# Optimization experiments

Hardware: AMD Instinct MI355X
Metric: run time of the kernel (lower is better)

The kernel has to match this reference:

```python
import jax, jax.numpy as jnp
import numpy as np

B, MB, NB, C = 4, 4096, 16384, 64

def setup_inputs() -> dict:
    key = jax.random.key(0)
    k1, k2, k3 = jax.random.split(key, 3)
    xyz = jax.random.normal(k1, (B * MB, 3), dtype=jnp.float32) * 10.0
    new_xyz = jax.random.normal(k2, (B * NB, 3), dtype=jnp.float32) * 10.0
    features = jax.random.normal(k3, (B * MB, C), dtype=jnp.float32)
    xyz_batch_cnt = jnp.full((B,), MB, dtype=jnp.int32)
    new_xyz_batch_cnt = jnp.full((B,), NB, dtype=jnp.int32)
    return {
        "xyz": xyz,
        "xyz_batch_cnt": xyz_batch_cnt,
        "new_xyz": new_xyz,
        "new_xyz_batch_cnt": new_xyz_batch_cnt,
        "features": features,
    }

def _three_nn_interp(query, known, feats):
    # query: (Nb,3), known: (Mb,3), feats: (Mb,C)
    # squared pairwise distances (Nb, Mb)
    d2 = (jnp.sum(query * query, -1, keepdims=True)
          - 2.0 * (query @ known.T)
          + jnp.sum(known * known, -1)[None, :])
    neg_d2, idx = jax.lax.top_k(-d2, 3)            # 3 nearest, (Nb,3)
    dist = jnp.sqrt(jnp.maximum(-neg_d2, 0.0))      # OpenPCDet returns sqrt(dist2)
    dist_recip = 1.0 / (dist + 1e-8)
    weight = dist_recip / jnp.sum(dist_recip, -1, keepdims=True)  # (Nb,3)
    gathered = feats[idx]                           # (Nb,3,C)
    return jnp.einsum('nkc,nk->nc', gathered, weight)

def reference(xyz, xyz_batch_cnt, new_xyz, new_xyz_batch_cnt, features):
    b = xyz_batch_cnt.shape[0]
    mb = xyz.shape[0] // b
    nb = new_xyz.shape[0] // b
    known_b = xyz.reshape(b, mb, 3)
    query_b = new_xyz.reshape(b, nb, 3)
    feats_b = features.reshape(b, mb, -1)
    out = jax.vmap(_three_nn_interp)(query_b, known_b, feats_b)  # (B,Nb,C)
    return out.reshape(b * nb, -1)
```

## Files before the change

kernel.cpp:

```cpp
#include <hip/hip_runtime.h>
#include <math.h>

#define NBIN   512
#define BEXT   64.0f
#define WSLACK 0.02f
#define AWIN   4.0f
#define SLC    64
#define BTH1   1024

__device__ __forceinline__ int bin1(float x) {
    int c = (int)floorf((x + BEXT) * 4.0f);
    return min(NBIN - 1, max(0, c));
}
__device__ __forceinline__ unsigned f2sort(float f) {
    int b = __float_as_int(f);
    return (unsigned)b ^ (0x80000000u | (unsigned)(b >> 31));
}
__device__ __forceinline__ float sort2f(unsigned u) {
    unsigned b = (u & 0x80000000u) ? (u ^ 0x80000000u) : ~u;
    return __uint_as_float(b);
}
__device__ __forceinline__ void ins3k(unsigned long long k,
                                      unsigned long long& k0,
                                      unsigned long long& k1,
                                      unsigned long long& k2) {
    const bool c0 = k < k0, c1 = k < k1, c2 = k < k2;
    k2 = c1 ? k1 : (c2 ? k : k2);
    k1 = c0 ? k0 : (c1 ? k : k1);
    k0 = c0 ? k  : k0;
}
__device__ __forceinline__ unsigned long long shfl_xor_u64(unsigned long long v, int m) {
    unsigned lo = (unsigned)v, hi = (unsigned)(v >> 32);
    lo = __shfl_xor((int)lo, m, 64);
    hi = __shfl_xor((int)hi, m, 64);
    return ((unsigned long long)hi << 32) | lo;
}

extern "C" __global__ void __launch_bounds__(256)
k_shist(const float* __restrict__ xyz, const float* __restrict__ nxyz,
        int B, int mb, int nb,
        int* __restrict__ hP, int* __restrict__ hQ, int* __restrict__ ovf_cnt)
{
    __shared__ int hist[NBIN];
    const int bid = (int)blockIdx.x;
    const bool isQ = bid >= B * SLC;
    const int rb = isQ ? bid - B * SLC : bid;
    const int b = rb / SLC, s = rb % SLC;
    const int n = isQ ? nb : mb;
    const int len = (n + SLC - 1) / SLC;
    const int beg = s * len, end = min(n, beg + len);
    const float* P = (isQ ? nxyz : xyz) + (size_t)b * n * 3;
    const int tid = threadIdx.x;

    if (bid == 0 && tid < B) ovf_cnt[tid] = 0;

    for (int i = tid; i < NBIN; i += 256) hist[i] = 0;
    __syncthreads();
    for (int i = beg + tid; i < end; i += 256) atomicAdd(&hist[bin1(P[i * 3])], 1);
    __syncthreads();
    int* dst = (isQ ? hQ : hP) + ((size_t)b * SLC + s) * NBIN;
    for (int i = tid; i < NBIN; i += 256) dst[i] = hist[i];
}

extern "C" __global__ void __launch_bounds__(NBIN)
k_sscan(int* __restrict__ hP, int* __restrict__ hQ,
        int* __restrict__ boff, int B, int mb)
{
    __shared__ int sc[NBIN];
    const bool isQ = (int)blockIdx.x >= B;
    const int b = isQ ? (int)blockIdx.x - B : (int)blockIdx.x;
    int* h = (isQ ? hQ : hP) + (size_t)b * SLC * NBIN;
    const int c = threadIdx.x;

    int run = 0;
    for (int s = 0; s < SLC; ++s) {
        const int v = h[s * NBIN + c];
        h[s * NBIN + c] = run;
        run += v;
    }
    sc[c] = run;
    __syncthreads();
    for (int off = 1; off < NBIN; off <<= 1) {
        const int t = (c >= off) ? sc[c - off] : 0;
        __syncthreads();
        sc[c] += t;
        __syncthreads();
    }
    const int excl = sc[c] - run;
    for (int s = 0; s < SLC; ++s) h[s * NBIN + c] += excl;
    if (!isQ) {
        boff[(size_t)b * (NBIN + 1) + c] = excl;
        if (c == NBIN - 1) boff[(size_t)b * (NBIN + 1) + NBIN] = mb;
    }
}

extern "C" __global__ void __launch_bounds__(256)
k_sscat(const float* __restrict__ xyz, const float* __restrict__ nxyz,
        int B, int mb, int nb,
        const int* __restrict__ hP, const int* __restrict__ hQ,
        float4* __restrict__ ps, int* __restrict__ pidx, int* __restrict__ qord)
{
    __shared__ int cur[NBIN];
    const int bid = (int)blockIdx.x;
    const bool isQ = bid >= B * SLC;
    const int rb = isQ ? bid - B * SLC : bid;
    const int b = rb / SLC, s = rb % SLC;
    const int n = isQ ? nb : mb;
    const int len = (n + SLC - 1) / SLC;
    const int beg = s * len, end = min(n, beg + len);
    const float* P = (isQ ? nxyz : xyz) + (size_t)b * n * 3;
    const int tid = threadIdx.x;
    const int* src = (isQ ? hQ : hP) + ((size_t)b * SLC + s) * NBIN;

    for (int i = tid; i < NBIN; i += 256) cur[i] = src[i];
    __syncthreads();
    for (int i = beg + tid; i < end; i += 256) {
        const float x = P[i * 3], y = P[i * 3 + 1], z = P[i * 3 + 2];
        const int pos = atomicAdd(&cur[bin1(x)], 1);
        if (isQ) {
            qord[(size_t)b * nb + pos] = i;
        } else {
            float pn;
            {
#pragma clang fp contract(off)
                pn = (x * x + y * y) + z * z;
            }
            ps[(size_t)b * mb + pos]   = make_float4(x, y, z, pn);
            pidx[(size_t)b * mb + pos] = i;
        }
    }
}

extern "C" __global__ void __launch_bounds__(BTH1)
build1d(const float* __restrict__ xyz, const float* __restrict__ nxyz,
        int mb, int nb,
        float4* __restrict__ ps, int* __restrict__ pidx,
        int* __restrict__ qord, int* __restrict__ boff,
        int* __restrict__ ovf_cnt)
{
    __shared__ int hist[NBIN];
    __shared__ int scanb[NBIN];
    const int B    = (int)gridDim.x / 2;
    const bool isQ = (int)blockIdx.x >= B;
    const int b    = isQ ? (int)blockIdx.x - B : (int)blockIdx.x;
    const int tid  = threadIdx.x;
    const int n    = isQ ? nb : mb;
    const float* P = (isQ ? nxyz : xyz) + (size_t)b * n * 3;

    if (blockIdx.x == 0 && tid < B) ovf_cnt[tid] = 0;

    if (tid < NBIN) hist[tid] = 0;
    __syncthreads();
    for (int i = tid; i < n; i += BTH1) atomicAdd(&hist[bin1(P[i * 3])], 1);
    __syncthreads();
    int h = 0;
    if (tid < NBIN) { h = hist[tid]; scanb[tid] = h; }
    __syncthreads();
    for (int off = 1; off < NBIN; off <<= 1) {
        int t = 0;
        if (tid < NBIN && tid >= off) t = scanb[tid - off];
        __syncthreads();
        if (tid < NBIN) scanb[tid] += t;
        __syncthreads();
    }
    if (tid < NBIN) {
        const int excl = scanb[tid] - h;
        if (!isQ) {
            boff[(size_t)b * (NBIN + 1) + tid] = excl;
            if (tid == NBIN - 1) boff[(size_t)b * (NBIN + 1) + NBIN] = n;
        }
        hist[tid] = excl;
    }
    __syncthreads();
    for (int i = tid; i < n; i += BTH1) {
        const float x = P[i * 3], y = P[i * 3 + 1], z = P[i * 3 + 2];
        const int c = bin1(x);
        const int pos = atomicAdd(&hist[c], 1);
        if (isQ) {
            qord[(size_t)b * nb + pos] = i;
        } else {
            float pn;
            {
#pragma clang fp contract(off)
                pn = (x * x + y * y) + z * z;
            }
            ps[(size_t)b * mb + pos]   = make_float4(x, y, z, pn);
            pidx[(size_t)b * mb + pos] = i;
        }
    }
}

#define QWA  8
#define SWA  8
#define WVBA 4
#define WTHA (WVBA * 64)
#define QPBA (WVBA * QWA)
#define CHA  64

extern "C" __global__ void __launch_bounds__(WTHA)
knn_phaseA(const float* __restrict__ nxyz, const float* __restrict__ feats,
           const int* __restrict__ qord, const int* __restrict__ boff,
           const float4* __restrict__ ps, const int* __restrict__ pidx,
           float* __restrict__ out, int* __restrict__ ovf, float* __restrict__ ovf_ub,
           int* __restrict__ ovf_cnt, int mb, int nb, int C)
{
    __shared__ float4 sP[WVBA][CHA];
    __shared__ int    sI[WVBA][CHA];

    const int tid  = threadIdx.x;
    const int w    = tid >> 6;
    const int l    = tid & 63;
    const int qi   = l & 7;
    const int side = l >> 3;
    const int wid  = blockIdx.x * WVBA + w;
    const int q0   = wid * QWA;
    const int b    = q0 / nb;

    const int qloc = qord[q0 + qi];
    const int row  = b * nb + qloc;
    const float qx = nxyz[(size_t)row * 3 + 0];
    const float qy = nxyz[(size_t)row * 3 + 1];
    const float qz = nxyz[(size_t)row * 3 + 2];
    float qq;
    {
#pragma clang fp contract(off)
        qq = (qx * qx + qy * qy) + qz * qz;
    }

    float mn = qx, mx = qx;
#pragma unroll
    for (int m = 1; m < 64; m <<= 1) {
        mn = fminf(mn, __shfl_xor(mn, m, 64));
        mx = fmaxf(mx, __shfl_xor(mx, m, 64));
    }

    const int*    boffb = boff + (size_t)b * (NBIN + 1);
    const float4* psb   = ps   + (size_t)b * mb;
    const int*    pib   = pidx + (size_t)b * mb;

    unsigned long long k0 = ~0ull, k1 = ~0ull, k2 = ~0ull;

    float4 rP;
    int    rI = 0;
    bool   rV = false;
    auto issue = [&](int base, int hi) {
        const int cand = base + l;
        rV = cand < hi;
        if (rV) { rP = psb[cand]; rI = pib[cand]; }
    };
    auto commit = [&]() {
        if (rV) { sP[w][l] = rP; sI[w][l] = rI; }
    };
    auto process = [&](int cnt) {
#pragma unroll
        for (int u = 0; u < CHA / SWA; ++u) {
            const int j = side + u * SWA;
            if (j < cnt) {
                const float4 Pt = sP[w][j];
                const int    pi = sI[w][j];
                const float dot = fmaf(qz, Pt.z, fmaf(qy, Pt.y, qx * Pt.x));
                const float d2  = fmaf(-2.0f, dot, qq) + Pt.w;
                const unsigned long long key =
                    ((unsigned long long)f2sort(d2) << 32) | (unsigned)pi;
                if (key < k2) {
                    const bool c0 = key < k0, c1 = key < k1;
                    k2 = c1 ? k1 : key;
                    k1 = c0 ? k0 : (c1 ? key : k1);
                    k0 = c0 ? key : k0;
                }
            }
        }
    };

    const int blo = bin1(mn - AWIN);
    const int bhi = bin1(mx + AWIN);
    {
        const int lo = boffb[blo], hi = boffb[bhi + 1];
        if (lo < hi) {
            issue(lo, hi);
            for (int base = lo; base < hi; base += CHA) {
                commit();
                if (base + CHA < hi) issue(base + CHA, hi);
                process(min(CHA, hi - base));
            }
        }
    }

    unsigned long long m0 = k0, m1 = k1, m2 = k2;
#pragma unroll
    for (int mk = 8; mk <= 32; mk <<= 1) {
        const unsigned long long t0 = shfl_xor_u64(m0, mk);
        const unsigned long long t1 = shfl_xor_u64(m1, mk);
        const unsigned long long t2 = shfl_xor_u64(m2, mk);
        ins3k(t0, m0, m1, m2); ins3k(t1, m0, m1, m2); ins3k(t2, m0, m1, m2);
    }

    const unsigned h2 = (unsigned)(m2 >> 32);
    const float ub = (h2 == 0xFFFFFFFFu) ? INFINITY : sort2f(h2);
    const float eL = fmaf(0.25f, (float)blo, -BEXT);
    const float eR = fmaf(0.25f, (float)(bhi + 1), -BEXT);
    const float gL = qx - eL;
    const float gR = eR - qx;
    const bool okL = (blo == 0)        || (gL * gL > ub + WSLACK);
    const bool okR = (bhi >= NBIN - 1) || (gR * gR > ub + WSLACK);
    const bool resolved = okL && okR && (h2 != 0xFFFFFFFFu);

    const bool need = (side == 0) && !resolved;
    const unsigned long long bm = __ballot(need);
    if (bm) {
        const int rank = __popcll(bm & ((1ull << l) - 1ull));
        const int tot  = __popcll(bm);
        const int lead = __ffsll((unsigned long long)bm) - 1;
        int base = 0;
        if (l == lead) base = atomicAdd(&ovf_cnt[b], tot);
        base = __shfl(base, lead, 64);
        if (need) {
            ovf[(size_t)b * nb + base + rank]    = row;
            ovf_ub[(size_t)b * nb + base + rank] = ub;
        }
    }

    const float d0  = sort2f((unsigned)(m0 >> 32));
    const float d1  = sort2f((unsigned)(m1 >> 32));
    const float d2v = sort2f((unsigned)(m2 >> 32));
    const float da = sqrtf(fmaxf(d0, 0.0f));
    const float db = sqrtf(fmaxf(d1, 0.0f));
    const float dc = sqrtf(fmaxf(d2v, 0.0f));
    const float ra = 1.0f / (da + 1e-8f);
    const float rb = 1.0f / (db + 1e-8f);
    const float rc = 1.0f / (dc + 1e-8f);
    float rs;
    {
#pragma clang fp contract(off)
        rs = (ra + rb) + rc;
    }
    const float wa = ra / rs, wb = rb / rs, wc = rc / rs;
    const int   ia = b * mb + (int)(unsigned)(m0 & 0xFFFFFFFFu);
    const int   ib = b * mb + (int)(unsigned)(m1 & 0xFFFFFFFFu);
    const int   ic = b * mb + (int)(unsigned)(m2 & 0xFFFFFFFFu);

    for (int q = 0; q < QWA; ++q) {
        if (__shfl((int)resolved, q, 64) == 0) continue;
        const float wa_ = __shfl(wa, q, 64);
        const float wb_ = __shfl(wb, q, 64);
        const float wc_ = __shfl(wc, q, 64);
        const int   ia_ = __shfl(ia, q, 64);
        const int   ib_ = __shfl(ib, q, 64);
        const int   ic_ = __shfl(ic, q, 64);
        const int   rw_ = __shfl(row, q, 64);
        const size_t ga = (size_t)ia_ * C;
        const size_t gb = (size_t)ib_ * C;
        const size_t gc = (size_t)ic_ * C;
        const size_t go = (size_t)rw_ * C;
        for (int ch = l; ch < C; ch += 64) {
            out[go + ch] = wa_ * feats[ga + ch] + wb_ * feats[gb + ch] + wc_ * feats[gc + ch];
        }
    }
}

#define WPBB 8
#define BTH2 (WPBB * 64)

extern "C" __global__ void __launch_bounds__(BTH2)
knn_phaseB2(const float* __restrict__ nxyz, const float* __restrict__ feats,
            const int* __restrict__ ovf, const float* __restrict__ ovf_ub,
            const int* __restrict__ ovf_cnt, const int* __restrict__ boff,
            const float4* __restrict__ ps, const int* __restrict__ pidx,
            float* __restrict__ out, int mb, int nb, int C)
{
    const int tid  = threadIdx.x;
    const int w    = tid >> 6;
    const int l    = tid & 63;
    const int bpb  = nb / WPBB;
    const int bb   = (int)blockIdx.x / bpb;
    const int slot = ((int)blockIdx.x % bpb) * WPBB + w;
    const int cnt  = ovf_cnt[bb];
    if (slot >= cnt) return;

    const int   row = ovf[(size_t)bb * nb + slot];
    const float ub  = ovf_ub[(size_t)bb * nb + slot];
    const float qx = nxyz[(size_t)row * 3 + 0];
    const float qy = nxyz[(size_t)row * 3 + 1];
    const float qz = nxyz[(size_t)row * 3 + 2];
    float qq;
    {
#pragma clang fp contract(off)
        qq = (qx * qx + qy * qy) + qz * qz;
    }

    int blo = 0, bhi = NBIN - 1;
    if (ub < 1e30f) {
        const float r = sqrtf(ub + 2.0f * WSLACK);
        blo = bin1(qx - r);
        bhi = bin1(qx + r);
    }
    const int*    boffb = boff + (size_t)bb * (NBIN + 1);
    const float4* psb   = ps   + (size_t)bb * mb;
    const int*    pib   = pidx + (size_t)bb * mb;
    const int lo = boffb[blo], hi = boffb[bhi + 1];

    unsigned long long k0 = ~0ull, k1 = ~0ull, k2 = ~0ull;
#pragma unroll 4
    for (int t = lo + l; t < hi; t += 64) {
        const float4 Pt = psb[t];
        const int    pi = pib[t];
        const float dot = fmaf(qz, Pt.z, fmaf(qy, Pt.y, qx * Pt.x));
        const float d2  = fmaf(-2.0f, dot, qq) + Pt.w;
        const unsigned long long key =
            ((unsigned long long)f2sort(d2) << 32) | (unsigned)pi;
        if (key < k2) {
            const bool c0 = key < k0, c1 = key < k1;
            k2 = c1 ? k1 : key;
            k1 = c0 ? k0 : (c1 ? key : k1);
            k0 = c0 ? key : k0;
        }
    }

#pragma unroll
    for (int m = 1; m < 64; m <<= 1) {
        const unsigned long long t0 = shfl_xor_u64(k0, m);
        const unsigned long long t1 = shfl_xor_u64(k1, m);
        const unsigned long long t2 = shfl_xor_u64(k2, m);
        ins3k(t0, k0, k1, k2); ins3k(t1, k0, k1, k2); ins3k(t2, k0, k1, k2);
    }

    const float d0  = sort2f((unsigned)(k0 >> 32));
    const float d1  = sort2f((unsigned)(k1 >> 32));
    const float d2v = sort2f((unsigned)(k2 >> 32));
    const float da = sqrtf(fmaxf(d0, 0.0f));
    const float db = sqrtf(fmaxf(d1, 0.0f));
    const float dc = sqrtf(fmaxf(d2v, 0.0f));
    const float ra = 1.0f / (da + 1e-8f);
    const float rb = 1.0f / (db + 1e-8f);
    const float rc = 1.0f / (dc + 1e-8f);
    float rs;
    {
#pragma clang fp contract(off)
        rs = (ra + rb) + rc;
    }
    const float wa = ra / rs, wb = rb / rs, wc = rc / rs;
    const size_t ga = (size_t)(bb * mb + (int)(unsigned)(k0 & 0xFFFFFFFFu)) * C;
    const size_t gb = (size_t)(bb * mb + (int)(unsigned)(k1 & 0xFFFFFFFFu)) * C;
    const size_t gc = (size_t)(bb * mb + (int)(unsigned)(k2 & 0xFFFFFFFFu)) * C;
    const size_t go = (size_t)row * C;
    for (int ch = l; ch < C; ch += 64) {
        out[go + ch] = wa * feats[ga + ch] + wb * feats[gb + ch] + wc * feats[gc + ch];
    }
}

#define THREADS 512
#define WAVES   8
#define RQ      2
#define QPB     128
#define CHUNK   2048

extern "C" __global__ void __launch_bounds__(THREADS)
knn3_v5(const float* __restrict__ xyz,
        const float* __restrict__ new_xyz,
        const float* __restrict__ feats,
        float* __restrict__ out,
        int mb, int nb, int C)
{
    extern __shared__ float smem[];
    float4* s_pts = (float4*)smem;
    const int tid = threadIdx.x;
    const int w   = tid >> 6;
    const int l   = tid & 63;
    const int block_q0 = blockIdx.x * QPB;
    const int batch    = block_q0 / nb;
    const int known0   = batch * mb;

    float qx[RQ], qy[RQ], qz[RQ], qq[RQ];
#pragma unroll
    for (int r = 0; r < RQ; ++r) {
        const int gq = block_q0 + r * 64 + l;
        qx[r] = new_xyz[(size_t)gq * 3 + 0];
        qy[r] = new_xyz[(size_t)gq * 3 + 1];
        qz[r] = new_xyz[(size_t)gq * 3 + 2];
        {
#pragma clang fp contract(off)
            qq[r] = (qx[r] * qx[r] + qy[r] * qy[r]) + qz[r] * qz[r];
        }
    }
    float b0[RQ], b1[RQ], b2[RQ];
    int   i0[RQ], i1[RQ], i2[RQ];
#pragma unroll
    for (int r = 0; r < RQ; ++r) {
        b0[r] = INFINITY; b1[r] = INFINITY; b2[r] = INFINITY;
        i0[r] = 0; i1[r] = 0; i2[r] = 0;
    }
    const int nch = (mb + CHUNK - 1) / CHUNK;
    for (int c = 0; c < nch; ++c) {
        const int base = c * CHUNK;
        const int cnt  = min(CHUNK, mb - base);
        if (c > 0) __syncthreads();
        const float* src = xyz + (size_t)(known0 + base) * 3;
        for (int p = tid; p < cnt; p += THREADS) {
            const float px = src[p * 3 + 0];
            const float py = src[p * 3 + 1];
            const float pz = src[p * 3 + 2];
            float pn;
            {
#pragma clang fp contract(off)
                pn = (px * px + py * py) + pz * pz;
            }
            s_pts[p] = make_float4(px, py, pz, pn);
        }
        __syncthreads();
        const int lo = (w * cnt) / WAVES;
        const int hi = ((w + 1) * cnt) / WAVES;
#pragma unroll 4
        for (int p = lo; p < hi; ++p) {
            const float4 P = s_pts[p];
            const int gp = base + p;
#pragma unroll
            for (int r = 0; r < RQ; ++r) {
                const float dot = fmaf(qz[r], P.z, fmaf(qy[r], P.y, qx[r] * P.x));
                const float d2  = fmaf(-2.0f, dot, qq[r]) + P.w;
                const bool c0 = d2 < b0[r];
                const bool c1 = d2 < b1[r];
                const bool c2 = d2 < b2[r];
                const float n0 = fminf(d2, b0[r]);
                const float n1 = __builtin_amdgcn_fmed3f(d2, b0[r], b1[r]);
                const float n2 = __builtin_amdgcn_fmed3f(d2, b1[r], b2[r]);
                const int  j0 = c0 ? gp : i0[r];
                const int  j1 = c0 ? i0[r] : (c1 ? gp : i1[r]);
                const int  j2 = c1 ? i1[r] : (c2 ? gp : i2[r]);
                b0[r] = n0; b1[r] = n1; b2[r] = n2;
                i0[r] = j0; i1[r] = j1; i2[r] = j2;
            }
        }
    }
    __syncthreads();
    float* sB  = smem;
    int*   sI  = (int*)smem + 3 * WAVES * QPB;
    float* sFW = smem + 6 * WAVES * QPB;
    int*   sFI = (int*)sFW + 3 * QPB;
#pragma unroll
    for (int r = 0; r < RQ; ++r) {
        const int qb = r * 64 + l;
        sB[(0 * WAVES + w) * QPB + qb] = b0[r];
        sB[(1 * WAVES + w) * QPB + qb] = b1[r];
        sB[(2 * WAVES + w) * QPB + qb] = b2[r];
        sI[(0 * WAVES + w) * QPB + qb] = i0[r];
        sI[(1 * WAVES + w) * QPB + qb] = i1[r];
        sI[(2 * WAVES + w) * QPB + qb] = i2[r];
    }
    __syncthreads();
    if (tid < QPB) {
        float mv0 = sB[(0 * WAVES) * QPB + tid];
        float mv1 = sB[(1 * WAVES) * QPB + tid];
        float mv2 = sB[(2 * WAVES) * QPB + tid];
        int   mi0 = sI[(0 * WAVES) * QPB + tid];
        int   mi1 = sI[(1 * WAVES) * QPB + tid];
        int   mi2 = sI[(2 * WAVES) * QPB + tid];
        for (int c = 1; c < WAVES; ++c) {
#pragma unroll
            for (int kk = 0; kk < 3; ++kk) {
                const float x  = sB[(kk * WAVES + c) * QPB + tid];
                const int   xi = sI[(kk * WAVES + c) * QPB + tid];
                const bool c0 = (x < mv0) || (x == mv0 && xi < mi0);
                const bool c1 = (x < mv1) || (x == mv1 && xi < mi1);
                const bool c2 = (x < mv2) || (x == mv2 && xi < mi2);
                const float n2 = c1 ? mv1 : (c2 ? x : mv2);
                const int   j2 = c1 ? mi1 : (c2 ? xi : mi2);
                const float n1 = c0 ? mv0 : (c1 ? x : mv1);
                const int   j1 = c0 ? mi0 : (c1 ? xi : mi1);
                const float n0 = c0 ? x : mv0;
                const int   j0 = c0 ? xi : mi0;
                mv0 = n0; mv1 = n1; mv2 = n2;
                mi0 = j0; mi1 = j1; mi2 = j2;
            }
        }
        const float da = sqrtf(fmaxf(mv0, 0.0f));
        const float db = sqrtf(fmaxf(mv1, 0.0f));
        const float dc = sqrtf(fmaxf(mv2, 0.0f));
        const float ra = 1.0f / (da + 1e-8f);
        const float rb = 1.0f / (db + 1e-8f);
        const float rc = 1.0f / (dc + 1e-8f);
        float rsum;
        {
#pragma clang fp contract(off)
            rsum = (ra + rb) + rc;
        }
        sFW[0 * QPB + tid] = ra / rsum;
        sFW[1 * QPB + tid] = rb / rsum;
        sFW[2 * QPB + tid] = rc / rsum;
        sFI[0 * QPB + tid] = known0 + mi0;
        sFI[1 * QPB + tid] = known0 + mi1;
        sFI[2 * QPB + tid] = known0 + mi2;
    }
    __syncthreads();
    const int qpw = QPB / WAVES;
    for (int j = 0; j < qpw; ++j) {
        const int qi2 = w * qpw + j;
        const float wa = sFW[0 * QPB + qi2];
        const float wb = sFW[1 * QPB + qi2];
        const float wc = sFW[2 * QPB + qi2];
        const size_t ga = (size_t)sFI[0 * QPB + qi2] * C;
        const size_t gb = (size_t)sFI[1 * QPB + qi2] * C;
        const size_t gc = (size_t)sFI[2 * QPB + qi2] * C;
        const size_t go = (size_t)(block_q0 + qi2) * C;
        for (int ch = l; ch < C; ch += 64) {
            out[go + ch] = wa * feats[ga + ch] + wb * feats[gb + ch] + wc * feats[gc + ch];
        }
    }
}

#define FQPB 256
extern "C" __global__ void __launch_bounds__(FQPB)
knn3_fallback(const float* __restrict__ xyz,
              const float* __restrict__ new_xyz,
              const float* __restrict__ feats,
              float* __restrict__ out,
              int mb, int nb, int C)
{
    extern __shared__ float4 s_pts[];
    const int tid      = threadIdx.x;
    const int block_q0 = blockIdx.x * FQPB;
    const int batch    = block_q0 / nb;
    const int known0   = batch * mb;
    for (int p = tid; p < mb; p += FQPB) {
        const float px = xyz[(size_t)(known0 + p) * 3 + 0];
        const float py = xyz[(size_t)(known0 + p) * 3 + 1];
        const float pz = xyz[(size_t)(known0 + p) * 3 + 2];
        float pn;
        {
#pragma clang fp contract(off)
            pn = (px * px + py * py) + pz * pz;
        }
        s_pts[p] = make_float4(px, py, pz, pn);
    }
    __syncthreads();
    const int gq = block_q0 + tid;
    const float qx = new_xyz[(size_t)gq * 3 + 0];
    const float qy = new_xyz[(size_t)gq * 3 + 1];
    const float qz = new_xyz[(size_t)gq * 3 + 2];
    float qq;
    {
#pragma clang fp contract(off)
        qq = (qx * qx + qy * qy) + qz * qz;
    }
    float b0 = INFINITY, b1 = INFINITY, b2 = INFINITY;
    int   i0 = 0, i1 = 0, i2 = 0;
#pragma unroll 8
    for (int p = 0; p < mb; ++p) {
        const float4 P = s_pts[p];
        const float dot = fmaf(qz, P.z, fmaf(qy, P.y, qx * P.x));
        const float d2  = fmaf(-2.0f, dot, qq) + P.w;
        const bool c0 = d2 < b0;
        const bool c1 = d2 < b1;
        const bool c2 = d2 < b2;
        b2 = c1 ? b1 : (c2 ? d2 : b2);
        i2 = c1 ? i1 : (c2 ? p  : i2);
        b1 = c0 ? b0 : (c1 ? d2 : b1);
        i1 = c0 ? i0 : (c1 ? p  : i1);
        b0 = c0 ? d2 : b0;
        i0 = c0 ? p  : i0;
    }
    const float da = sqrtf(fmaxf(b0, 0.0f));
    const float db = sqrtf(fmaxf(b1, 0.0f));
    const float dc = sqrtf(fmaxf(b2, 0.0f));
    const float ra = 1.0f / (da + 1e-8f);
    const float rb = 1.0f / (db + 1e-8f);
    const float rc = 1.0f / (dc + 1e-8f);
    float rsum;
    {
#pragma clang fp contract(off)
        rsum = (ra + rb) + rc;
    }
    const float wa = ra / rsum, wb = rb / rsum, wc = rc / rsum;
    const size_t ga = (size_t)(known0 + i0) * C;
    const size_t gb = (size_t)(known0 + i1) * C;
    const size_t gc = (size_t)(known0 + i2) * C;
    const size_t go = (size_t)gq * C;
    for (int ch = 0; ch < C; ++ch) {
        out[go + ch] = wa * feats[ga + ch] + wb * feats[gb + ch] + wc * feats[gc + ch];
    }
}

extern "C" void kernel_launch(void* const* d_in, const int* in_sizes, int n_in,
                              void* d_out, int out_size, void* d_ws, size_t ws_size,
                              hipStream_t stream) {
    const float* xyz     = (const float*)d_in[0];
    const float* new_xyz = (const float*)d_in[2];
    const float* feats   = (const float*)d_in[4];
    float*       out     = (float*)d_out;

    const int n_known = in_sizes[0] / 3;
    const int B       = in_sizes[1];
    const int n_query = in_sizes[2] / 3;
    const int C       = in_sizes[4] / n_known;
    const int mb      = n_known / B;
    const int nb      = n_query / B;

    char* wp = (char*)d_ws;
    float4* ps      = (float4*)wp;  wp += (size_t)B * mb * sizeof(float4);
    int*    pidx    = (int*)wp;     wp += (size_t)B * mb * sizeof(int);
    int*    qord    = (int*)wp;     wp += (size_t)B * nb * sizeof(int);
    int*    boff    = (int*)wp;     wp += (size_t)B * (NBIN + 1) * sizeof(int);
    int*    ovf     = (int*)wp;     wp += (size_t)B * nb * sizeof(int);
    float*  ovf_ub  = (float*)wp;   wp += (size_t)B * nb * sizeof(float);
    int*    ovf_cnt = (int*)wp;     wp += (size_t)B * sizeof(int);
    const size_t need_base = (size_t)(wp - (char*)d_ws);
    int*    hP      = (int*)wp;     wp += (size_t)B * SLC * NBIN * sizeof(int);
    int*    hQ      = (int*)wp;     wp += (size_t)B * SLC * NBIN * sizeof(int);
    const size_t need_slice = (size_t)(wp - (char*)d_ws);

    const bool ok_shape = (nb % QWA) == 0 && (n_query % QPBA) == 0 &&
                          (nb % WPBB) == 0 && mb >= 3 && B <= 256;

    if (ok_shape && ws_size >= need_slice) {
        k_shist<<<2 * B * SLC, 256, 0, stream>>>(xyz, new_xyz, B, mb, nb, hP, hQ, ovf_cnt);
        k_sscan<<<2 * B, NBIN, 0, stream>>>(hP, hQ, boff, B, mb);
        k_sscat<<<2 * B * SLC, 256, 0, stream>>>(xyz, new_xyz, B, mb, nb, hP, hQ,
                                                 ps, pidx, qord);
        knn_phaseA<<<n_query / QPBA, WTHA, 0, stream>>>(
            new_xyz, feats, qord, boff, ps, pidx, out, ovf, ovf_ub, ovf_cnt,
            mb, nb, C);
        knn_phaseB2<<<B * (nb / WPBB), BTH2, 0, stream>>>(
            new_xyz, feats, ovf, ovf_ub, ovf_cnt, boff, ps, pidx, out, mb, nb, C);
    } else if (ok_shape && ws_size >= need_base && B <= BTH1) {
        build1d<<<2 * B, BTH1, 0, stream>>>(xyz, new_xyz, mb, nb, ps, pidx, qord,
                                            boff, ovf_cnt);
        knn_phaseA<<<n_query / QPBA, WTHA, 0, stream>>>(
            new_xyz, feats, qord, boff, ps, pidx, out, ovf, ovf_ub, ovf_cnt,
            mb, nb, C);
        knn_phaseB2<<<B * (nb / WPBB), BTH2, 0, stream>>>(
            new_xyz, feats, ovf, ovf_ub, ovf_cnt, boff, ps, pidx, out, mb, nb, C);
    } else if ((nb % QPB) == 0) {
        const size_t smem_chunk = (size_t)CHUNK * sizeof(float4);
        const size_t smem_merge = (size_t)(6 * WAVES * QPB + 6 * QPB) * sizeof(float);
        const size_t shmem = smem_chunk > smem_merge ? smem_chunk : smem_merge;
        knn3_v5<<<n_query / QPB, THREADS, shmem, stream>>>(
            xyz, new_xyz, feats, out, mb, nb, C);
    } else {
        const size_t shmem = (size_t)mb * sizeof(float4);
        knn3_fallback<<<(n_query + FQPB - 1) / FQPB, FQPB, shmem, stream>>>(
            xyz, new_xyz, feats, out, mb, nb, C);
    }
}
```

Baseline: 97.00 us.

## Replace 1D x-binning with 2D x/y grid for candidate search

```diff
diff --git a/kernel.cpp b/kernel.cpp
--- a/kernel.cpp
+++ b/kernel.cpp
@@ -1,16 +1,24 @@
 #include <hip/hip_runtime.h>
 #include <math.h>
 
-#define NBIN   512
-#define BEXT   64.0f
+#define NXB    256
+#define NYS    32
+#define NB2    (NYS * NXB)
 #define WSLACK 0.02f
-#define AWIN   4.0f
-#define SLC    64
-#define BTH1   1024
-
-__device__ __forceinline__ int bin1(float x) {
-    int c = (int)floorf((x + BEXT) * 4.0f);
-    return min(NBIN - 1, max(0, c));
+#define WX     3.0f
+#define WY     3.0f
+#define SLC2   8
+
+__device__ __forceinline__ int xbin(float x) {
+    int c = (int)floorf((x + 64.0f) * 2.0f);
+    return min(NXB - 1, max(0, c));
+}
+__device__ __forceinline__ int ybin(float y) {
+    int c = (int)floorf((y + 64.0f) * 0.25f);
+    return min(NYS - 1, max(0, c));
+}
+__device__ __forceinline__ int key2(float x, float y) {
+    return ybin(y) * NXB + xbin(x);
 }
 __device__ __forceinline__ unsigned f2sort(float f) {
     int b = __float_as_int(f);
@@ -37,86 +45,99 @@
 }
 
 extern "C" __global__ void __launch_bounds__(256)
-k_shist(const float* __restrict__ xyz, const float* __restrict__ nxyz,
-        int B, int mb, int nb,
-        int* __restrict__ hP, int* __restrict__ hQ, int* __restrict__ ovf_cnt)
+k_shist2(const float* __restrict__ xyz, const float* __restrict__ nxyz,
+         int B, int mb, int nb,
+         int* __restrict__ hP, int* __restrict__ hQ, int* __restrict__ ovf_cnt)
 {
-    __shared__ int hist[NBIN];
+    __shared__ int hist[NB2];
     const int bid = (int)blockIdx.x;
-    const bool isQ = bid >= B * SLC;
-    const int rb = isQ ? bid - B * SLC : bid;
-    const int b = rb / SLC, s = rb % SLC;
+    const bool isQ = bid >= B * SLC2;
+    const int rb = isQ ? bid - B * SLC2 : bid;
+    const int b = rb / SLC2, s = rb % SLC2;
     const int n = isQ ? nb : mb;
-    const int len = (n + SLC - 1) / SLC;
+    const int len = (n + SLC2 - 1) / SLC2;
     const int beg = s * len, end = min(n, beg + len);
     const float* P = (isQ ? nxyz : xyz) + (size_t)b * n * 3;
     const int tid = threadIdx.x;
 
     if (bid == 0 && tid < B) ovf_cnt[tid] = 0;
 
-    for (int i = tid; i < NBIN; i += 256) hist[i] = 0;
-    __syncthreads();
-    for (int i = beg + tid; i < end; i += 256) atomicAdd(&hist[bin1(P[i * 3])], 1);
-    __syncthreads();
-    int* dst = (isQ ? hQ : hP) + ((size_t)b * SLC + s) * NBIN;
-    for (int i = tid; i < NBIN; i += 256) dst[i] = hist[i];
-}
-
-extern "C" __global__ void __launch_bounds__(NBIN)
-k_sscan(int* __restrict__ hP, int* __restrict__ hQ,
-        int* __restrict__ boff, int B, int mb)
+    for (int i = tid; i < NB2; i += 256) hist[i] = 0;
+    __syncthreads();
+    for (int i = beg + tid; i < end; i += 256)
+        atomicAdd(&hist[key2(P[i * 3], P[i * 3 + 1])], 1);
+    __syncthreads();
+    int* dst = (isQ ? hQ : hP) + ((size_t)b * SLC2 + s) * NB2;
+    for (int i = tid; i < NB2; i += 256) dst[i] = hist[i];
+}
+
+extern "C" __global__ void __launch_bounds__(512)
+k_sscan2(int* __restrict__ hP, int* __restrict__ hQ,
+         int* __restrict__ boff, int B, int mb)
 {
-    __shared__ int sc[NBIN];
+    __shared__ int ts[512];
     const bool isQ = (int)blockIdx.x >= B;
     const int b = isQ ? (int)blockIdx.x - B : (int)blockIdx.x;
-    int* h = (isQ ? hQ : hP) + (size_t)b * SLC * NBIN;
-    const int c = threadIdx.x;
-
-    int run = 0;
-    for (int s = 0; s < SLC; ++s) {
-        const int v = h[s * NBIN + c];
-        h[s * NBIN + c] = run;
-        run += v;
-    }
-    sc[c] = run;
-    __syncthreads();
-    for (int off = 1; off < NBIN; off <<= 1) {
-        const int t = (c >= off) ? sc[c - off] : 0;
+    int* h = (isQ ? hQ : hP) + (size_t)b * SLC2 * NB2;
+    const int t = threadIdx.x;
+
+    int tot[16];
+    int tsum = 0;
+#pragma unroll
+    for (int j = 0; j < 16; ++j) {
+        const int c = t * 16 + j;
+        int run = 0;
+        for (int s = 0; s < SLC2; ++s) {
+            const int v = h[s * NB2 + c];
+            h[s * NB2 + c] = run;
+            run += v;
+        }
+        tot[j] = run;
+        tsum += run;
+    }
+    ts[t] = tsum;
+    __syncthreads();
+    for (int off = 1; off < 512; off <<= 1) {
+        const int v = (t >= off) ? ts[t - off] : 0;
         __syncthreads();
-        sc[c] += t;
+        ts[t] += v;
         __syncthreads();
     }
-    const int excl = sc[c] - run;
-    for (int s = 0; s < SLC; ++s) h[s * NBIN + c] += excl;
-    if (!isQ) {
-        boff[(size_t)b * (NBIN + 1) + c] = excl;
-        if (c == NBIN - 1) boff[(size_t)b * (NBIN + 1) + NBIN] = mb;
-    }
+    int excl = ts[t] - tsum;
+#pragma unroll
+    for (int j = 0; j < 16; ++j) {
+        const int c = t * 16 + j;
+        const int e = excl;
+        excl += tot[j];
+        for (int s = 0; s < SLC2; ++s) h[s * NB2 + c] += e;
+        if (!isQ) boff[(size_t)b * (NB2 + 1) + c] = e;
+    }
+    if (!isQ && t == 511) boff[(size_t)b * (NB2 + 1) + NB2] = mb;
 }
 
 extern "C" __global__ void __launch_bounds__(256)
-k_sscat(const float* __restrict__ xyz, const float* __restrict__ nxyz,
-        int B, int mb, int nb,
-        const int* __restrict__ hP, const int* __restrict__ hQ,
-        float4* __restrict__ ps, int* __restrict__ pidx, int* __restrict__ qord)
+k_sscat2(const float* __restrict__ xyz, const float* __restrict__ nxyz,
+         int B, int mb, int nb,
+         const int* __restrict__ hP, const int* __restrict__ hQ,
+         float4* __restrict__ ps, int* __restrict__ pidx, int* __restrict__ qord)
 {
-    __shared__ int cur[NBIN];
+    __shared__ int cur[NB2];
     const int bid = (int)blockIdx.x;
-    const bool isQ = bid >= B * SLC;
-    const int rb = isQ ? bid - B * SLC : bid;
-    const int b = rb / SLC, s = rb % SLC;
+    const bool isQ = bid >= B * SLC2;
+    const int rb = isQ ? bid - B * SLC2 : bid;
+    const int b = rb / SLC2, s = rb % SLC2;
     const int n = isQ ? nb : mb;
-    const int len = (n + SLC - 1) / SLC;
+    const int len = (n + SLC2 - 1) / SLC2;
     const int beg = s * len, end = min(n, beg + len);
     const float* P = (isQ ? nxyz : xyz) + (size_t)b * n * 3;
     const int tid = threadIdx.x;
-    const int* src = (isQ ? hQ : hP) + ((size_t)b * SLC + s) * NBIN;
-
-    for (int i = tid; i < NBIN; i += 256) cur[i] = src[i];
+    const int* src = (isQ ? hQ : hP) + ((size_t)b * SLC2 + s) * NB2;
+
+    for (int i = tid; i < NB2; i += 256) cur[i] = src[i];
     __syncthreads();
     for (int i = beg + tid; i < end; i += 256) {
         const float x = P[i * 3], y = P[i * 3 + 1], z = P[i * 3 + 2];
-        const int pos = atomicAdd(&cur[bin1(x)], 1);
+        const int pos = atomicAdd(&cur[key2(x, y)], 1);
         if (isQ) {
             qord[(size_t)b * nb + pos] = i;
         } else {
@@ -131,15 +152,15 @@
     }
 }
 
-extern "C" __global__ void __launch_bounds__(BTH1)
-build1d(const float* __restrict__ xyz, const float* __restrict__ nxyz,
+extern "C" __global__ void __launch_bounds__(1024)
+build2d(const float* __restrict__ xyz, const float* __restrict__ nxyz,
         int mb, int nb,
         float4* __restrict__ ps, int* __restrict__ pidx,
         int* __restrict__ qord, int* __restrict__ boff,
         int* __restrict__ ovf_cnt)
 {
-    __shared__ int hist[NBIN];
-    __shared__ int scanb[NBIN];
+    extern __shared__ int hist[];
+    __shared__ int ts[1024];
     const int B    = (int)gridDim.x / 2;
     const bool isQ = (int)blockIdx.x >= B;
     const int b    = isQ ? (int)blockIdx.x - B : (int)blockIdx.x;
@@ -149,33 +170,40 @@
 
     if (blockIdx.x == 0 && tid < B) ovf_cnt[tid] = 0;
 
-    if (tid < NBIN) hist[tid] = 0;
-    __syncthreads();
-    for (int i = tid; i < n; i += BTH1) atomicAdd(&hist[bin1(P[i * 3])], 1);
-    __syncthreads();
-    int h = 0;
-    if (tid < NBIN) { h = hist[tid]; scanb[tid] = h; }
-    __syncthreads();
-    for (int off = 1; off < NBIN; off <<= 1) {
-        int t = 0;
-        if (tid < NBIN && tid >= off) t = scanb[tid - off];
+    for (int i = tid; i < NB2; i += 1024) hist[i] = 0;
+    __syncthreads();
+    for (int i = tid; i < n; i += 1024)
+        atomicAdd(&hist[key2(P[i * 3], P[i * 3 + 1])], 1);
+    __syncthreads();
+    int tot[8];
+    int tsum = 0;
+#pragma unroll
+    for (int j = 0; j < 8; ++j) {
+        tot[j] = hist[tid * 8 + j];
+        tsum += tot[j];
+    }
+    ts[tid] = tsum;
+    __syncthreads();
+    for (int off = 1; off < 1024; off <<= 1) {
+        const int v = (tid >= off) ? ts[tid - off] : 0;
         __syncthreads();
-        if (tid < NBIN) scanb[tid] += t;
+        ts[tid] += v;
         __syncthreads();
     }
-    if (tid < NBIN) {
-        const int excl = scanb[tid] - h;
-        if (!isQ) {
-            boff[(size_t)b * (NBIN + 1) + tid] = excl;
-            if (tid == NBIN - 1) boff[(size_t)b * (NBIN + 1) + NBIN] = n;
-        }
-        hist[tid] = excl;
-    }
-    __syncthreads();
-    for (int i = tid; i < n; i += BTH1) {
+    int excl = ts[tid] - tsum;
+#pragma unroll
+    for (int j = 0; j < 8; ++j) {
+        const int c = tid * 8 + j;
+        const int e = excl;
+        excl += tot[j];
+        hist[c] = e;
+        if (!isQ) boff[(size_t)b * (NB2 + 1) + c] = e;
+    }
+    if (!isQ && tid == 1023) boff[(size_t)b * (NB2 + 1) + NB2] = mb;
+    __syncthreads();
+    for (int i = tid; i < n; i += 1024) {
         const float x = P[i * 3], y = P[i * 3 + 1], z = P[i * 3 + 2];
-        const int c = bin1(x);
-        const int pos = atomicAdd(&hist[c], 1);
+        const int pos = atomicAdd(&hist[key2(x, y)], 1);
         if (isQ) {
             qord[(size_t)b * nb + pos] = i;
         } else {
@@ -227,14 +255,16 @@
         qq = (qx * qx + qy * qy) + qz * qz;
     }
 
-    float mn = qx, mx = qx;
+    float mnx = qx, mxx = qx, mny = qy, mxy = qy;
 #pragma unroll
     for (int m = 1; m < 64; m <<= 1) {
-        mn = fminf(mn, __shfl_xor(mn, m, 64));
-        mx = fmaxf(mx, __shfl_xor(mx, m, 64));
-    }
-
-    const int*    boffb = boff + (size_t)b * (NBIN + 1);
+        mnx = fminf(mnx, __shfl_xor(mnx, m, 64));
+        mxx = fmaxf(mxx, __shfl_xor(mxx, m, 64));
+        mny = fminf(mny, __shfl_xor(mny, m, 64));
+        mxy = fmaxf(mxy, __shfl_xor(mxy, m, 64));
+    }
+
+    const int*    boffb = boff + (size_t)b * (NB2 + 1);
     const float4* psb   = ps   + (size_t)b * mb;
     const int*    pib   = pidx + (size_t)b * mb;
 
@@ -249,42 +279,41 @@
         if (rV) { rP = psb[cand]; rI = pib[cand]; }
     };
     auto commit = [&]() {
-        if (rV) { sP[w][l] = rP; sI[w][l] = rI; }
+        sP[w][l] = rV ? rP : make_float4(0.0f, 0.0f, 0.0f, INFINITY);
+        sI[w][l] = rV ? rI : 0;
     };
-    auto process = [&](int cnt) {
+    auto process = [&]() {
 #pragma unroll
         for (int u = 0; u < CHA / SWA; ++u) {
             const int j = side + u * SWA;
-            if (j < cnt) {
-                const float4 Pt = sP[w][j];
-                const int    pi = sI[w][j];
-                const float dot = fmaf(qz, Pt.z, fmaf(qy, Pt.y, qx * Pt.x));
-                const float d2  = fmaf(-2.0f, dot, qq) + Pt.w;
-                const unsigned long long key =
-                    ((unsigned long long)f2sort(d2) << 32) | (unsigned)pi;
-                if (key < k2) {
-                    const bool c0 = key < k0, c1 = key < k1;
-                    k2 = c1 ? k1 : key;
-                    k1 = c0 ? k0 : (c1 ? key : k1);
-                    k0 = c0 ? key : k0;
-                }
+            const float4 Pt = sP[w][j];
+            const int    pi = sI[w][j];
+            const float dot = fmaf(qz, Pt.z, fmaf(qy, Pt.y, qx * Pt.x));
+            const float d2  = fmaf(-2.0f, dot, qq) + Pt.w;
+            const unsigned long long key =
+                ((unsigned long long)f2sort(d2) << 32) | (unsigned)pi;
+            if (key < k2) {
+                const bool c0 = key < k0, c1 = key < k1;
+                k2 = c1 ? k1 : key;
+                k1 = c0 ? k0 : (c1 ? key : k1);
+                k0 = c0 ? key : k0;
             }
         }
     };
-
-    const int blo = bin1(mn - AWIN);
-    const int bhi = bin1(mx + AWIN);
-    {
-        const int lo = boffb[blo], hi = boffb[bhi + 1];
-        if (lo < hi) {
-            issue(lo, hi);
-            for (int base = lo; base < hi; base += CHA) {
-                commit();
-                if (base + CHA < hi) issue(base + CHA, hi);
-                process(min(CHA, hi - base));
-            }
-        }
-    }
+    auto scan = [&](int lo, int hi) {
+        if (lo >= hi) return;
+        issue(lo, hi);
+        for (int base = lo; base < hi; base += CHA) {
+            commit();
+            if (base + CHA < hi) issue(base + CHA, hi);
+            process();
+        }
+    };
+
+    const int ys_lo = ybin(mny - WY), ys_hi = ybin(mxy + WY);
+    const int xb_lo = xbin(mnx - WX), xb_hi = xbin(mxx + WX);
+    for (int s = ys_lo; s <= ys_hi; ++s)
+        scan(boffb[s * NXB + xb_lo], boffb[s * NXB + xb_hi + 1]);
 
     unsigned long long m0 = k0, m1 = k1, m2 = k2;
 #pragma unroll
@@ -297,13 +326,18 @@
 
     const unsigned h2 = (unsigned)(m2 >> 32);
     const float ub = (h2 == 0xFFFFFFFFu) ? INFINITY : sort2f(h2);
-    const float eL = fmaf(0.25f, (float)blo, -BEXT);
-    const float eR = fmaf(0.25f, (float)(bhi + 1), -BEXT);
-    const float gL = qx - eL;
-    const float gR = eR - qx;
-    const bool okL = (blo == 0)        || (gL * gL > ub + WSLACK);
-    const bool okR = (bhi >= NBIN - 1) || (gR * gR > ub + WSLACK);
-    const bool resolved = okL && okR && (h2 != 0xFFFFFFFFu);
+    const float eLx = fmaf(0.5f, (float)xb_lo,       -64.0f);
+    const float eRx = fmaf(0.5f, (float)(xb_hi + 1), -64.0f);
+    const float eLy = fmaf(4.0f, (float)ys_lo,       -64.0f);
+    const float eRy = fmaf(4.0f, (float)(ys_hi + 1), -64.0f);
+    const float gXL = qx - eLx, gXR = eRx - qx;
+    const float gYL = qy - eLy, gYR = eRy - qy;
+    const bool okXL = (xb_lo == 0)        || (gXL * gXL > ub + WSLACK);
+    const bool okXR = (xb_hi >= NXB - 1)  || (gXR * gXR > ub + WSLACK);
+    const bool okYL = (ys_lo == 0)        || (gYL * gYL > ub + WSLACK);
+    const bool okYR = (ys_hi >= NYS - 1)  || (gYR * gYR > ub + WSLACK);
+    const bool resolved = okXL && okXR && okYL && okYR &&
+                          (h2 != 0xFFFFFFFFu) && (ub < 1e30f);
 
     const bool need = (side == 0) && !resolved;
     const unsigned long long bm = __ballot(need);
@@ -388,31 +422,34 @@
         qq = (qx * qx + qy * qy) + qz * qz;
     }
 
-    int blo = 0, bhi = NBIN - 1;
+    int ysl = 0, ysh = NYS - 1, xbl = 0, xbh = NXB - 1;
     if (ub < 1e30f) {
         const float r = sqrtf(ub + 2.0f * WSLACK);
-        blo = bin1(qx - r);
-        bhi = bin1(qx + r);
-    }
-    const int*    boffb = boff + (size_t)bb * (NBIN + 1);
+        ysl = ybin(qy - r); ysh = ybin(qy + r);
+        xbl = xbin(qx - r); xbh = xbin(qx + r);
+    }
+    const int*    boffb = boff + (size_t)bb * (NB2 + 1);
     const float4* psb   = ps   + (size_t)bb * mb;
     const int*    pib   = pidx + (size_t)bb * mb;
-    const int lo = boffb[blo], hi = boffb[bhi + 1];
 
     unsigned long long k0 = ~0ull, k1 = ~0ull, k2 = ~0ull;
+    for (int s = ysl; s <= ysh; ++s) {
+        const int lo = boffb[s * NXB + xbl];
+        const int hi = boffb[s * NXB + xbh + 1];
 #pragma unroll 4
-    for (int t = lo + l; t < hi; t += 64) {
-        const float4 Pt = psb[t];
-        const int    pi = pib[t];
-        const float dot = fmaf(qz, Pt.z, fmaf(qy, Pt.y, qx * Pt.x));
-        const float d2  = fmaf(-2.0f, dot, qq) + Pt.w;
-        const unsigned long long key =
-            ((unsigned long long)f2sort(d2) << 32) | (unsigned)pi;
-        if (key < k2) {
-            const bool c0 = key < k0, c1 = key < k1;
-            k2 = c1 ? k1 : key;
-            k1 = c0 ? k0 : (c1 ? key : k1);
-            k0 = c0 ? key : k0;
+        for (int t = lo + l; t < hi; t += 64) {
+            const float4 Pt = psb[t];
+            const int    pi = pib[t];
+            const float dot = fmaf(qz, Pt.z, fmaf(qy, Pt.y, qx * Pt.x));
+            const float d2  = fmaf(-2.0f, dot, qq) + Pt.w;
+            const unsigned long long key =
+                ((unsigned long long)f2sort(d2) << 32) | (unsigned)pi;
+            if (key < k2) {
+                const bool c0 = key < k0, c1 = key < k1;
+                k2 = c1 ? k1 : key;
+                k1 = c0 ? k0 : (c1 ? key : k1);
+                k0 = c0 ? key : k0;
+            }
         }
     }
 
@@ -698,31 +735,32 @@
     float4* ps      = (float4*)wp;  wp += (size_t)B * mb * sizeof(float4);
     int*    pidx    = (int*)wp;     wp += (size_t)B * mb * sizeof(int);
     int*    qord    = (int*)wp;     wp += (size_t)B * nb * sizeof(int);
-    int*    boff    = (int*)wp;     wp += (size_t)B * (NBIN + 1) * sizeof(int);
+    int*    boff    = (int*)wp;     wp += (size_t)B * (NB2 + 1) * sizeof(int);
     int*    ovf     = (int*)wp;     wp += (size_t)B * nb * sizeof(int);
     float*  ovf_ub  = (float*)wp;   wp += (size_t)B * nb * sizeof(float);
     int*    ovf_cnt = (int*)wp;     wp += (size_t)B * sizeof(int);
     const size_t need_base = (size_t)(wp - (char*)d_ws);
-    int*    hP      = (int*)wp;     wp += (size_t)B * SLC * NBIN * sizeof(int);
-    int*    hQ      = (int*)wp;     wp += (size_t)B * SLC * NBIN * sizeof(int);
+    int*    hP      = (int*)wp;     wp += (size_t)B * SLC2 * NB2 * sizeof(int);
+    int*    hQ      = (int*)wp;     wp += (size_t)B * SLC2 * NB2 * sizeof(int);
     const size_t need_slice = (size_t)(wp - (char*)d_ws);
 
     const bool ok_shape = (nb % QWA) == 0 && (n_query % QPBA) == 0 &&
                           (nb % WPBB) == 0 && mb >= 3 && B <= 256;
 
     if (ok_shape && ws_size >= need_slice) {
-        k_shist<<<2 * B * SLC, 256, 0, stream>>>(xyz, new_xyz, B, mb, nb, hP, hQ, ovf_cnt);
-        k_sscan<<<2 * B, NBIN, 0, stream>>>(hP, hQ, boff, B, mb);
-        k_sscat<<<2 * B * SLC, 256, 0, stream>>>(xyz, new_xyz, B, mb, nb, hP, hQ,
-                                                 ps, pidx, qord);
+        k_shist2<<<2 * B * SLC2, 256, 0, stream>>>(xyz, new_xyz, B, mb, nb,
+                                                   hP, hQ, ovf_cnt);
+        k_sscan2<<<2 * B, 512, 0, stream>>>(hP, hQ, boff, B, mb);
+        k_sscat2<<<2 * B * SLC2, 256, 0, stream>>>(xyz, new_xyz, B, mb, nb,
+                                                   hP, hQ, ps, pidx, qord);
         knn_phaseA<<<n_query / QPBA, WTHA, 0, stream>>>(
             new_xyz, feats, qord, boff, ps, pidx, out, ovf, ovf_ub, ovf_cnt,
             mb, nb, C);
         knn_phaseB2<<<B * (nb / WPBB), BTH2, 0, stream>>>(
             new_xyz, feats, ovf, ovf_ub, ovf_cnt, boff, ps, pidx, out, mb, nb, C);
-    } else if (ok_shape && ws_size >= need_base && B <= BTH1) {
-        build1d<<<2 * B, BTH1, 0, stream>>>(xyz, new_xyz, mb, nb, ps, pidx, qord,
-                                            boff, ovf_cnt);
+    } else if (ok_shape && ws_size >= need_base && B <= 1024) {
+        build2d<<<2 * B, 1024, (size_t)NB2 * sizeof(int), stream>>>(
+            xyz, new_xyz, mb, nb, ps, pidx, qord, boff, ovf_cnt);
         knn_phaseA<<<n_query / QPBA, WTHA, 0, stream>>>(
             new_xyz, feats, qord, boff, ps, pidx, out, ovf, ovf_ub, ovf_cnt,
             mb, nb, C);
```

Measured after the change: 203.0 us. 2.09x slower.
